# Kernel tuning notes

Hardware: AMD Instinct MI355X
Metric: run time of the kernel (lower is better)

The kernel has to match this reference:

```python
import jax, jax.numpy as jnp
import numpy as np

B, N, D = 32, 256, 3
NF, L = 16, 3


def _fully_connected(n):
    # Same ordering as connect_fully: for i in range(n) for j in range(n) if i != j
    a = np.repeat(np.arange(n), n)
    b = np.tile(np.arange(n), n)
    m = a != b
    return a[m].astype(np.int32), b[m].astype(np.int32)


def setup_inputs() -> dict:
    key = jax.random.key(0)
    ks = jax.random.split(key, 12)
    src, dst = _fully_connected(N)
    s = 0.1  # small param scale for numerical stability
    return {
        "xs": jax.random.normal(ks[0], (B, N, D), jnp.float32),
        "vs": jax.random.normal(ks[1], (B, N, D), jnp.float32),
        "charges": jax.random.normal(ks[2], (B * N, 1), jnp.float32),
        "W_in": s * jax.random.normal(ks[3], (1, NF), jnp.float32),
        "b_in": jnp.zeros((NF,), jnp.float32),
        "W_v": s * jax.random.normal(ks[4], (L, NF, 1), jnp.float32),
        "We1": s * jax.random.normal(ks[5], (L, 2 * NF + 1, NF), jnp.float32),
        "be1": jnp.zeros((L, NF), jnp.float32),
        "We2": s * jax.random.normal(ks[6], (L, NF, NF), jnp.float32),
        "be2": jnp.zeros((L, NF), jnp.float32),
        "Wx": s * jax.random.normal(ks[7], (L, NF, 1), jnp.float32),
        "Wh1": s * jax.random.normal(ks[8], (L, 2 * NF, NF), jnp.float32),
        "bh1": jnp.zeros((L, NF), jnp.float32),
        "src": jnp.asarray(src),
        "dst": jnp.asarray(dst),
    }


def reference(xs, vs, charges, W_in, b_in, W_v, We1, be1, We2, be2, Wx, Wh1, bh1, src, dst):
    b, n, d = xs.shape
    # node scalar features from charges (ndata['f'])
    h = jax.nn.relu(charges.reshape(b, n, 1) @ W_in + b_in)  # [B,N,nf]
    x = xs
    n_layers = We1.shape[0]
    for l in range(n_layers):
        # fully-connected edge gather + subtract (edata['d'])
        de = x[:, dst] - x[:, src]                         # [B,E,3]
        r2 = jnp.sum(de * de, axis=-1, keepdims=True)      # [B,E,1]
        e_in = jnp.concatenate([h[:, src], h[:, dst], r2], axis=-1)  # [B,E,2nf+1]
        m = jax.nn.relu(e_in @ We1[l] + be1[l])
        m = jax.nn.relu(m @ We2[l] + be2[l])               # [B,E,nf]
        w = m @ Wx[l]                                      # [B,E,1]
        # equivariant coordinate update: scatter-add edge vectors into dst nodes
        agg_x = jnp.zeros_like(x).at[:, dst].add(de * w) / (n - 1)
        x = x + agg_x + vs * (h @ W_v[l])                  # velocity term (ndata['vel'])
        m_agg = jnp.zeros_like(h).at[:, dst].add(m)        # [B,N,nf]
        h = h + jax.nn.relu(jnp.concatenate([h, m_agg], axis=-1) @ Wh1[l] + bh1[l])
    # OurDynamics returns (se3_out['1'] + xs).view(-1, n_dimension)
    return x.reshape(-1, d)
```

## Files before the change

kernel.cpp:

```cpp
#include <hip/hip_runtime.h>

#define BB 32
#define NN 256
#define NF 16

typedef _Float16 half4 __attribute__((ext_vector_type(4)));
typedef float f32x4 __attribute__((ext_vector_type(4)));

#define X0_OFF 0
#define X1_OFF 32768
#define H0_OFF 65536
#define H1_OFF 196608
#define SU0_OFF 327680
#define SV0_OFF 458752
#define SU1_OFF 589824
#define SV1_OFF 720896
#define SU2_OFF 851968
#define SV2_OFF 983040

__device__ __forceinline__ float dot4(float4 a, float4 b, float acc) {
    acc = fmaf(a.x, b.x, acc); acc = fmaf(a.y, b.y, acc);
    acc = fmaf(a.z, b.z, acc); acc = fmaf(a.w, b.w, acc);
    return acc;
}

__global__ __launch_bounds__(256)
void init_kernel(const float* __restrict__ xs, const float* __restrict__ charges,
                 const float* __restrict__ W_in, const float* __restrict__ b_in,
                 const float* __restrict__ We1, const float* __restrict__ be1,
                 float* __restrict__ x0, float* __restrict__ h0,
                 float* __restrict__ su0, float* __restrict__ sv0) {
    __shared__ float sWs[256], sWd[256];
    __shared__ __align__(16) float sh[16][NF];
    __shared__ float sb1[NF];
    const int tid = threadIdx.x;
    const size_t n0 = (size_t)blockIdx.x * 16;
    const int nl = tid >> 4;
    const int k  = tid & 15;
    sWs[tid] = We1[tid];
    sWd[tid] = We1[256 + tid];
    if (tid < NF) sb1[tid] = be1[tid];
    {
        const float c = charges[n0 + nl];
        const float hf = fmaxf(fmaf(c, W_in[k], b_in[k]), 0.f);
        sh[nl][k] = hf;
        h0[(n0 + nl) * NF + k] = hf;
    }
    if (tid < 64) {
        const int jd = tid >> 2, q = tid & 3;
        x0[(n0 + jd) * 4 + q] = (q < 3) ? xs[(n0 + jd) * 3 + q] : 0.f;
    }
    __syncthreads();
    {
        const float4* hn = (const float4*)&sh[nl][0];
        const float4 h0q = hn[0], h1q = hn[1], h2q = hn[2], h3q = hn[3];
        float u = 0.f, v = sb1[k];
#pragma unroll
        for (int q = 0; q < 4; ++q) {
            const float4 hq = (q == 0) ? h0q : (q == 1) ? h1q : (q == 2) ? h2q : h3q;
            u = fmaf(hq.x, sWs[(4 * q + 0) * NF + k], u);
            u = fmaf(hq.y, sWs[(4 * q + 1) * NF + k], u);
            u = fmaf(hq.z, sWs[(4 * q + 2) * NF + k], u);
            u = fmaf(hq.w, sWs[(4 * q + 3) * NF + k], u);
            v = fmaf(hq.x, sWd[(4 * q + 0) * NF + k], v);
            v = fmaf(hq.y, sWd[(4 * q + 1) * NF + k], v);
            v = fmaf(hq.z, sWd[(4 * q + 2) * NF + k], v);
            v = fmaf(hq.w, sWd[(4 * q + 3) * NF + k], v);
        }
        su0[(n0 + nl) * NF + k] = u;
        sv0[(n0 + nl) * NF + k] = v;
    }
}

__global__ __launch_bounds__(256)
void layer_kernel(const float* __restrict__ x_in, const float* __restrict__ h_in,
                  const float* __restrict__ su_in, const float* __restrict__ sv_in,
                  float* __restrict__ x_out, float* __restrict__ h_out,
                  float* __restrict__ su_out, float* __restrict__ sv_out,
                  const float* __restrict__ vs, const float* __restrict__ Wv_l,
                  const float* __restrict__ We1_l, const float* __restrict__ We2_l,
                  const float* __restrict__ be2_l, const float* __restrict__ Wx_l,
                  const float* __restrict__ Wh1_l, const float* __restrict__ bh1_l,
                  const float* __restrict__ We1_n, const float* __restrict__ be1_n,
                  int final_layer) {
    __shared__ __align__(16) float sSU[NN * NF];
    __shared__ __align__(16) float sX[NN * 4];
    __shared__ float sWh1s[512];
    __shared__ float sWa[256];
    __shared__ float sWb[256];
    __shared__ float sbe1n[NF];
    __shared__ float sh_new[8][NF + 1];
    __shared__ float sg[8][NF];

    const int tid  = threadIdx.x;
    const int b    = blockIdx.x >> 5;
    const int oct  = blockIdx.x & 31;
    const int n0l  = 8 * oct;
    const size_t n0 = (size_t)b * NN + n0l;
    const int w    = tid >> 6;
    const int lane = tid & 63;
    const int c    = lane & 15;
    const int g    = lane >> 4;

    sWh1s[tid]       = Wh1_l[tid];
    sWh1s[256 + tid] = Wh1_l[256 + tid];
    if (!final_layer) {
        const int f = tid >> 4, k = tid & 15;
        sWa[k * NF + f] = We1_n[tid];
        sWb[k * NF + f] = We1_n[256 + tid];
        if (tid < NF) sbe1n[tid] = be1_n[tid];
    }

    {
        const float4* gsu = (const float4*)(su_in + (size_t)b * NN * NF);
        float4* lsu = (float4*)sSU;
        lsu[tid]        = gsu[tid];
        lsu[256 + tid]  = gsu[256 + tid];
        lsu[512 + tid]  = gsu[512 + tid];
        lsu[768 + tid]  = gsu[768 + tid];
        const float4* gx = (const float4*)(x_in + (size_t)b * NN * 4);
        ((float4*)sX)[tid] = gx[tid];
    }
    __syncthreads();

    const int j0 = n0l + w, j1 = n0l + 4 + w;
    const float4 xj0 = *(const float4*)&sX[4 * j0];
    const float4 xj1 = *(const float4*)&sX[4 * j1];
    half4 afrag;
    afrag.x = (_Float16)We2_l[(4 * g + 0) * NF + c];
    afrag.y = (_Float16)We2_l[(4 * g + 1) * NF + c];
    afrag.z = (_Float16)We2_l[(4 * g + 2) * NF + c];
    afrag.w = (_Float16)We2_l[(4 * g + 3) * NF + c];
    const float4 v40  = *(const float4*)(sv_in + ((size_t)b * NN + j0) * NF + 4 * g);
    const float4 v41  = *(const float4*)(sv_in + ((size_t)b * NN + j1) * NF + 4 * g);
    const float4 wr4  = *(const float4*)(We1_l + 512 + 4 * g);
    const float4 be2f = *(const float4*)(be2_l + 4 * g);
    const float4 wxf  = *(const float4*)(Wx_l + 4 * g);
    f32x4 cb;
    cb.x = be2f.x; cb.y = be2f.y; cb.z = be2f.z; cb.w = be2f.w;

    float Sw0 = 0.f, Swx0 = 0.f, Swy0 = 0.f, Swz0 = 0.f;
    float Sw1 = 0.f, Swx1 = 0.f, Swy1 = 0.f, Swz1 = 0.f;
    float g00 = 0.f, g01 = 0.f, g02 = 0.f, g03 = 0.f;
    float g10 = 0.f, g11 = 0.f, g12 = 0.f, g13 = 0.f;

    const float* su_l = &sSU[c * NF + 4 * g];
    const float* x_l  = &sX[4 * c];

#pragma unroll 2
    for (int t = 0; t < 16; ++t) {
        const float4 u4  = *(const float4*)(su_l + 256 * t);
        const float4 xs4 = *(const float4*)(x_l + 64 * t);
        const int s = 16 * t + c;
        {
            const float dx = xj0.x - xs4.x, dy = xj0.y - xs4.y, dz = xj0.z - xs4.z;
            const float r2 = fmaf(dx, dx, fmaf(dy, dy, dz * dz));
            const float m0 = fmaxf(fmaf(r2, wr4.x, u4.x + v40.x), 0.f);
            const float m1 = fmaxf(fmaf(r2, wr4.y, u4.y + v40.y), 0.f);
            const float m2 = fmaxf(fmaf(r2, wr4.z, u4.z + v40.z), 0.f);
            const float m3 = fmaxf(fmaf(r2, wr4.w, u4.w + v40.w), 0.f);
            half4 bfrag;
            bfrag.x = (_Float16)m0; bfrag.y = (_Float16)m1;
            bfrag.z = (_Float16)m2; bfrag.w = (_Float16)m3;
            const f32x4 acc = __builtin_amdgcn_mfma_f32_16x16x16f16(afrag, bfrag, cb, 0, 0, 0);
            const float e0 = fmaxf(acc.x, 0.f);
            const float e1 = fmaxf(acc.y, 0.f);
            const float e2 = fmaxf(acc.z, 0.f);
            const float e3 = fmaxf(acc.w, 0.f);
            float wp = e0 * wxf.x;
            wp = fmaf(e1, wxf.y, wp);
            wp = fmaf(e2, wxf.z, wp);
            wp = fmaf(e3, wxf.w, wp);
            const float gsel = (s != j0) ? 1.f : 0.f;
            g00 = fmaf(e0, gsel, g00);
            g01 = fmaf(e1, gsel, g01);
            g02 = fmaf(e2, gsel, g02);
            g03 = fmaf(e3, gsel, g03);
            Sw0 += wp;
            Swx0 = fmaf(wp, xs4.x, Swx0);
            Swy0 = fmaf(wp, xs4.y, Swy0);
            Swz0 = fmaf(wp, xs4.z, Swz0);
        }
        {
            const float dx = xj1.x - xs4.x, dy = xj1.y - xs4.y, dz = xj1.z - xs4.z;
            const float r2 = fmaf(dx, dx, fmaf(dy, dy, dz * dz));
            const float m0 = fmaxf(fmaf(r2, wr4.x, u4.x + v41.x), 0.f);
            const float m1 = fmaxf(fmaf(r2, wr4.y, u4.y + v41.y), 0.f);
            const float m2 = fmaxf(fmaf(r2, wr4.z, u4.z + v41.z), 0.f);
            const float m3 = fmaxf(fmaf(r2, wr4.w, u4.w + v41.w), 0.f);
            half4 bfrag;
            bfrag.x = (_Float16)m0; bfrag.y = (_Float16)m1;
            bfrag.z = (_Float16)m2; bfrag.w = (_Float16)m3;
            const f32x4 acc = __builtin_amdgcn_mfma_f32_16x16x16f16(afrag, bfrag, cb, 0, 0, 0);
            const float e0 = fmaxf(acc.x, 0.f);
            const float e1 = fmaxf(acc.y, 0.f);
            const float e2 = fmaxf(acc.z, 0.f);
            const float e3 = fmaxf(acc.w, 0.f);
            float wp = e0 * wxf.x;
            wp = fmaf(e1, wxf.y, wp);
            wp = fmaf(e2, wxf.z, wp);
            wp = fmaf(e3, wxf.w, wp);
            const float gsel = (s != j1) ? 1.f : 0.f;
            g10 = fmaf(e0, gsel, g10);
            g11 = fmaf(e1, gsel, g11);
            g12 = fmaf(e2, gsel, g12);
            g13 = fmaf(e3, gsel, g13);
            Sw1 += wp;
            Swx1 = fmaf(wp, xs4.x, Swx1);
            Swy1 = fmaf(wp, xs4.y, Swy1);
            Swz1 = fmaf(wp, xs4.z, Swz1);
        }
    }

#pragma unroll
    for (int off = 1; off < 64; off <<= 1) {
        Sw0  += __shfl_xor(Sw0,  off, 64);  Sw1  += __shfl_xor(Sw1,  off, 64);
        Swx0 += __shfl_xor(Swx0, off, 64);  Swx1 += __shfl_xor(Swx1, off, 64);
        Swy0 += __shfl_xor(Swy0, off, 64);  Swy1 += __shfl_xor(Swy1, off, 64);
        Swz0 += __shfl_xor(Swz0, off, 64);  Swz1 += __shfl_xor(Swz1, off, 64);
    }
#pragma unroll
    for (int off = 1; off < 16; off <<= 1) {
        g00 += __shfl_xor(g00, off, 64);  g10 += __shfl_xor(g10, off, 64);
        g01 += __shfl_xor(g01, off, 64);  g11 += __shfl_xor(g11, off, 64);
        g02 += __shfl_xor(g02, off, 64);  g12 += __shfl_xor(g12, off, 64);
        g03 += __shfl_xor(g03, off, 64);  g13 += __shfl_xor(g13, off, 64);
    }
    if ((lane & 15) == 0) {
        *(float4*)&sg[w][4 * g]     = make_float4(g00, g01, g02, g03);
        *(float4*)&sg[w + 4][4 * g] = make_float4(g10, g11, g12, g13);
    }
    __syncthreads();

    const int is0 = (lane < 16);
    const int is1 = (lane >= 32 && lane < 48);
    if (is0 || is1) {
        const int f = lane & 15;
        const int slot = is0 ? w : (w + 4);
        const int jm   = is0 ? j0 : j1;
        const float SwS = is0 ? Sw0  : Sw1;
        const float SxS = is0 ? Swx0 : Swx1;
        const float SyS = is0 ? Swy0 : Swy1;
        const float SzS = is0 ? Swz0 : Swz1;
        const float4 xjm = is0 ? xj0 : xj1;
        const size_t nj = (size_t)b * NN + jm;
        float hd = bh1_l[f];
        float hv = 0.f;
#pragma unroll
        for (int k = 0; k < NF; ++k) {
            const float hjk = h_in[nj * NF + k];
            hd = fmaf(hjk, sWh1s[k * NF + f], hd);
            hv = fmaf(hjk, Wv_l[k], hv);
        }
#pragma unroll
        for (int k = 0; k < NF; ++k) {
            hd = fmaf(sg[slot][k], sWh1s[(NF + k) * NF + f], hd);
        }
        const float hnew = h_in[nj * NF + f] + fmaxf(hd, 0.f);
        sh_new[slot][f] = hnew;
        if (!final_layer) h_out[nj * NF + f] = hnew;
        if (f < 3) {
            const float xc = (f == 0) ? xjm.x : ((f == 1) ? xjm.y : xjm.z);
            const float Sc = (f == 0) ? SxS  : ((f == 1) ? SyS  : SzS);
            const float agg = (SwS * xc - Sc) * (1.f / 255.f);
            const float xnew = xc + agg + vs[nj * 3 + f] * hv;
            if (final_layer) x_out[nj * 3 + f] = xnew;
            else             x_out[nj * 4 + f] = xnew;
        }
        if (!final_layer && f == 3) x_out[nj * 4 + 3] = 0.f;
    }

    if (!final_layer) {
        __syncthreads();
        if (tid < 128) {
            const int jd = tid >> 4, k = tid & 15;
            float u = 0.f, v = sbe1n[k];
#pragma unroll
            for (int f = 0; f < NF; ++f) {
                const float hf = sh_new[jd][f];
                u = fmaf(hf, sWa[k * NF + f], u);
                v = fmaf(hf, sWb[k * NF + f], v);
            }
            su_out[(n0 + jd) * NF + k] = u;
            sv_out[(n0 + jd) * NF + k] = v;
        }
    }
}

extern "C" void kernel_launch(void* const* d_in, const int* in_sizes, int n_in,
                              void* d_out, int out_size, void* d_ws, size_t ws_size,
                              hipStream_t stream) {
    const float* xs      = (const float*)d_in[0];
    const float* vs      = (const float*)d_in[1];
    const float* charges = (const float*)d_in[2];
    const float* W_in    = (const float*)d_in[3];
    const float* b_in    = (const float*)d_in[4];
    const float* W_v     = (const float*)d_in[5];
    const float* We1     = (const float*)d_in[6];
    const float* be1     = (const float*)d_in[7];
    const float* We2     = (const float*)d_in[8];
    const float* be2     = (const float*)d_in[9];
    const float* Wx      = (const float*)d_in[10];
    const float* Wh1     = (const float*)d_in[11];
    const float* bh1     = (const float*)d_in[12];

    float* ws = (float*)d_ws;
    float* x0  = ws + X0_OFF;
    float* x1  = ws + X1_OFF;
    float* h0  = ws + H0_OFF;
    float* h1  = ws + H1_OFF;
    float* su0 = ws + SU0_OFF;
    float* sv0 = ws + SV0_OFF;
    float* su1 = ws + SU1_OFF;
    float* sv1 = ws + SV1_OFF;
    float* su2 = ws + SU2_OFF;
    float* sv2 = ws + SV2_OFF;
    float* out = (float*)d_out;

    hipLaunchKernelGGL(init_kernel, dim3(512), dim3(256), 0, stream,
                       xs, charges, W_in, b_in, We1, be1, x0, h0, su0, sv0);
    hipLaunchKernelGGL(layer_kernel, dim3(1024), dim3(256), 0, stream,
                       x0, h0, su0, sv0, x1, h1, su1, sv1,
                       vs, W_v + 0 * 16, We1 + 0 * 528, We2 + 0 * 256,
                       be2 + 0 * 16, Wx + 0 * 16, Wh1 + 0 * 512, bh1 + 0 * 16,
                       We1 + 1 * 528, be1 + 1 * 16, 0);
    hipLaunchKernelGGL(layer_kernel, dim3(1024), dim3(256), 0, stream,
                       x1, h1, su1, sv1, x0, h0, su2, sv2,
                       vs, W_v + 1 * 16, We1 + 1 * 528, We2 + 1 * 256,
                       be2 + 1 * 16, Wx + 1 * 16, Wh1 + 1 * 512, bh1 + 1 * 16,
                       We1 + 2 * 528, be1 + 2 * 16, 0);
    hipLaunchKernelGGL(layer_kernel, dim3(1024), dim3(256), 0, stream,
                       x0, h0, su2, sv2, out, h1, su1, sv1,
                       vs, W_v + 2 * 16, We1 + 2 * 528, We2 + 2 * 256,
                       be2 + 2 * 16, Wx + 2 * 16, Wh1 + 2 * 512, bh1 + 2 * 16,
                       We1 + 2 * 528, be1 + 2 * 16, 1);
}
```

Baseline: 132.8 us.

## Fuse init kernel into first layer kernel, recomputing node projections per block

```diff
diff --git a/kernel.cpp b/kernel.cpp
--- a/kernel.cpp
+++ b/kernel.cpp
@@ -1,93 +1,39 @@
 #include <hip/hip_runtime.h>
 
-#define BB 32
 #define NN 256
 #define NF 16
 
 typedef _Float16 half4 __attribute__((ext_vector_type(4)));
 typedef float f32x4 __attribute__((ext_vector_type(4)));
 
-#define X0_OFF 0
-#define X1_OFF 32768
-#define H0_OFF 65536
-#define H1_OFF 196608
-#define SU0_OFF 327680
-#define SV0_OFF 458752
-#define SU1_OFF 589824
-#define SV1_OFF 720896
-#define SU2_OFF 851968
-#define SV2_OFF 983040
-
-__device__ __forceinline__ float dot4(float4 a, float4 b, float acc) {
-    acc = fmaf(a.x, b.x, acc); acc = fmaf(a.y, b.y, acc);
-    acc = fmaf(a.z, b.z, acc); acc = fmaf(a.w, b.w, acc);
-    return acc;
-}
+#define XA_OFF 0
+#define XB_OFF 32768
+#define HA_OFF 65536
+#define HB_OFF 196608
+#define SUA_OFF 327680
+#define SVA_OFF 458752
+#define SUB_OFF 589824
+#define SVB_OFF 720896
 
 __global__ __launch_bounds__(256)
-void init_kernel(const float* __restrict__ xs, const float* __restrict__ charges,
-                 const float* __restrict__ W_in, const float* __restrict__ b_in,
-                 const float* __restrict__ We1, const float* __restrict__ be1,
-                 float* __restrict__ x0, float* __restrict__ h0,
-                 float* __restrict__ su0, float* __restrict__ sv0) {
-    __shared__ float sWs[256], sWd[256];
-    __shared__ __align__(16) float sh[16][NF];
-    __shared__ float sb1[NF];
-    const int tid = threadIdx.x;
-    const size_t n0 = (size_t)blockIdx.x * 16;
-    const int nl = tid >> 4;
-    const int k  = tid & 15;
-    sWs[tid] = We1[tid];
-    sWd[tid] = We1[256 + tid];
-    if (tid < NF) sb1[tid] = be1[tid];
-    {
-        const float c = charges[n0 + nl];
-        const float hf = fmaxf(fmaf(c, W_in[k], b_in[k]), 0.f);
-        sh[nl][k] = hf;
-        h0[(n0 + nl) * NF + k] = hf;
-    }
-    if (tid < 64) {
-        const int jd = tid >> 2, q = tid & 3;
-        x0[(n0 + jd) * 4 + q] = (q < 3) ? xs[(n0 + jd) * 3 + q] : 0.f;
-    }
-    __syncthreads();
-    {
-        const float4* hn = (const float4*)&sh[nl][0];
-        const float4 h0q = hn[0], h1q = hn[1], h2q = hn[2], h3q = hn[3];
-        float u = 0.f, v = sb1[k];
-#pragma unroll
-        for (int q = 0; q < 4; ++q) {
-            const float4 hq = (q == 0) ? h0q : (q == 1) ? h1q : (q == 2) ? h2q : h3q;
-            u = fmaf(hq.x, sWs[(4 * q + 0) * NF + k], u);
-            u = fmaf(hq.y, sWs[(4 * q + 1) * NF + k], u);
-            u = fmaf(hq.z, sWs[(4 * q + 2) * NF + k], u);
-            u = fmaf(hq.w, sWs[(4 * q + 3) * NF + k], u);
-            v = fmaf(hq.x, sWd[(4 * q + 0) * NF + k], v);
-            v = fmaf(hq.y, sWd[(4 * q + 1) * NF + k], v);
-            v = fmaf(hq.z, sWd[(4 * q + 2) * NF + k], v);
-            v = fmaf(hq.w, sWd[(4 * q + 3) * NF + k], v);
-        }
-        su0[(n0 + nl) * NF + k] = u;
-        sv0[(n0 + nl) * NF + k] = v;
-    }
-}
-
-__global__ __launch_bounds__(256)
-void layer_kernel(const float* __restrict__ x_in, const float* __restrict__ h_in,
-                  const float* __restrict__ su_in, const float* __restrict__ sv_in,
-                  float* __restrict__ x_out, float* __restrict__ h_out,
-                  float* __restrict__ su_out, float* __restrict__ sv_out,
-                  const float* __restrict__ vs, const float* __restrict__ Wv_l,
-                  const float* __restrict__ We1_l, const float* __restrict__ We2_l,
-                  const float* __restrict__ be2_l, const float* __restrict__ Wx_l,
-                  const float* __restrict__ Wh1_l, const float* __restrict__ bh1_l,
-                  const float* __restrict__ We1_n, const float* __restrict__ be1_n,
-                  int final_layer) {
+void layer0_kernel(const float* __restrict__ xs, const float* __restrict__ vs,
+                   const float* __restrict__ charges,
+                   const float* __restrict__ W_in, const float* __restrict__ b_in,
+                   const float* __restrict__ W_v, const float* __restrict__ We1_l,
+                   const float* __restrict__ be1_l, const float* __restrict__ We2_l,
+                   const float* __restrict__ be2_l, const float* __restrict__ Wx_l,
+                   const float* __restrict__ Wh1_l, const float* __restrict__ bh1_l,
+                   const float* __restrict__ We1_n, const float* __restrict__ be1_n,
+                   float* __restrict__ x_out, float* __restrict__ h_out,
+                   float* __restrict__ su_out, float* __restrict__ sv_out) {
     __shared__ __align__(16) float sSU[NN * NF];
     __shared__ __align__(16) float sX[NN * 4];
+    __shared__ __align__(16) float sHg[64 * NF];
+    __shared__ float sWs[256], sWd[256];
+    __shared__ __align__(16) float sSV8[8][NF];
+    __shared__ __align__(16) float sH8[8][NF + 1];
     __shared__ float sWh1s[512];
-    __shared__ float sWa[256];
-    __shared__ float sWb[256];
+    __shared__ float sWa[256], sWb[256];
     __shared__ float sbe1n[NF];
     __shared__ float sh_new[8][NF + 1];
     __shared__ float sg[8][NF];
@@ -102,26 +48,71 @@
     const int c    = lane & 15;
     const int g    = lane >> 4;
 
+    sWs[tid] = We1_l[tid];
+    sWd[tid] = We1_l[256 + tid];
     sWh1s[tid]       = Wh1_l[tid];
     sWh1s[256 + tid] = Wh1_l[256 + tid];
-    if (!final_layer) {
-        const int f = tid >> 4, k = tid & 15;
-        sWa[k * NF + f] = We1_n[tid];
-        sWb[k * NF + f] = We1_n[256 + tid];
+    {
+        const int f = tid >> 4, kk = tid & 15;
+        sWa[kk * NF + f] = We1_n[tid];
+        sWb[kk * NF + f] = We1_n[256 + tid];
         if (tid < NF) sbe1n[tid] = be1_n[tid];
     }
-
     {
-        const float4* gsu = (const float4*)(su_in + (size_t)b * NN * NF);
-        float4* lsu = (float4*)sSU;
-        lsu[tid]        = gsu[tid];
-        lsu[256 + tid]  = gsu[256 + tid];
-        lsu[512 + tid]  = gsu[512 + tid];
-        lsu[768 + tid]  = gsu[768 + tid];
-        const float4* gx = (const float4*)(x_in + (size_t)b * NN * 4);
-        ((float4*)sX)[tid] = gx[tid];
-    }
-    __syncthreads();
+        const size_t base = ((size_t)b * NN + tid) * 3;
+        sX[tid * 4 + 0] = xs[base + 0];
+        sX[tid * 4 + 1] = xs[base + 1];
+        sX[tid * 4 + 2] = xs[base + 2];
+        sX[tid * 4 + 3] = 0.f;
+    }
+
+    const int nl = tid >> 4, k = tid & 15;
+    const float win  = W_in[k];
+    const float bin  = b_in[k];
+    const float be1k = be1_l[k];
+    const int i0 = n0l >> 6;
+    const int r0 = (n0l & 63) >> 4;
+    const int halfsel = (n0l >> 3) & 1;
+    const int own = ((nl >> 3) == halfsel);
+#pragma unroll
+    for (int i = 0; i < 4; ++i) {
+#pragma unroll
+        for (int r = 0; r < 4; ++r) {
+            const float cq = charges[(size_t)b * NN + 64 * i + 16 * r + nl];
+            const float hf = fmaxf(fmaf(cq, win, bin), 0.f);
+            sHg[(16 * r + nl) * NF + k] = hf;
+            if (i == i0 && r == r0 && own) sH8[nl & 7][k] = hf;
+        }
+        __syncthreads();
+#pragma unroll
+        for (int r = 0; r < 4; ++r) {
+            const float4* hn = (const float4*)&sHg[(16 * r + nl) * NF];
+            const float4 h0q = hn[0], h1q = hn[1], h2q = hn[2], h3q = hn[3];
+            float u = 0.f;
+#pragma unroll
+            for (int q = 0; q < 4; ++q) {
+                const float4 hq = (q == 0) ? h0q : (q == 1) ? h1q : (q == 2) ? h2q : h3q;
+                u = fmaf(hq.x, sWs[(4 * q + 0) * NF + k], u);
+                u = fmaf(hq.y, sWs[(4 * q + 1) * NF + k], u);
+                u = fmaf(hq.z, sWs[(4 * q + 2) * NF + k], u);
+                u = fmaf(hq.w, sWs[(4 * q + 3) * NF + k], u);
+            }
+            sSU[(64 * i + 16 * r + nl) * NF + k] = u;
+            if (i == i0 && r == r0 && own) {
+                float v = be1k;
+#pragma unroll
+                for (int q = 0; q < 4; ++q) {
+                    const float4 hq = (q == 0) ? h0q : (q == 1) ? h1q : (q == 2) ? h2q : h3q;
+                    v = fmaf(hq.x, sWd[(4 * q + 0) * NF + k], v);
+                    v = fmaf(hq.y, sWd[(4 * q + 1) * NF + k], v);
+                    v = fmaf(hq.z, sWd[(4 * q + 2) * NF + k], v);
+                    v = fmaf(hq.w, sWd[(4 * q + 3) * NF + k], v);
+                }
+                sSV8[nl & 7][k] = v;
+            }
+        }
+        __syncthreads();
+    }
 
     const int j0 = n0l + w, j1 = n0l + 4 + w;
     const float4 xj0 = *(const float4*)&sX[4 * j0];
@@ -131,8 +122,8 @@
     afrag.y = (_Float16)We2_l[(4 * g + 1) * NF + c];
     afrag.z = (_Float16)We2_l[(4 * g + 2) * NF + c];
     afrag.w = (_Float16)We2_l[(4 * g + 3) * NF + c];
-    const float4 v40  = *(const float4*)(sv_in + ((size_t)b * NN + j0) * NF + 4 * g);
-    const float4 v41  = *(const float4*)(sv_in + ((size_t)b * NN + j1) * NF + 4 * g);
+    const float4 v40 = *(const float4*)&sSV8[w][4 * g];
+    const float4 v41 = *(const float4*)&sSV8[4 + w][4 * g];
     const float4 wr4  = *(const float4*)(We1_l + 512 + 4 * g);
     const float4 be2f = *(const float4*)(be2_l + 4 * g);
     const float4 wxf  = *(const float4*)(Wx_l + 4 * g);
@@ -247,6 +238,217 @@
         float hd = bh1_l[f];
         float hv = 0.f;
 #pragma unroll
+        for (int kk = 0; kk < NF; ++kk) {
+            const float hjk = sH8[slot][kk];
+            hd = fmaf(hjk, sWh1s[kk * NF + f], hd);
+            hv = fmaf(hjk, W_v[kk], hv);
+        }
+#pragma unroll
+        for (int kk = 0; kk < NF; ++kk) {
+            hd = fmaf(sg[slot][kk], sWh1s[(NF + kk) * NF + f], hd);
+        }
+        const float hnew = sH8[slot][f] + fmaxf(hd, 0.f);
+        sh_new[slot][f] = hnew;
+        h_out[nj * NF + f] = hnew;
+        if (f < 3) {
+            const float xc = (f == 0) ? xjm.x : ((f == 1) ? xjm.y : xjm.z);
+            const float Sc = (f == 0) ? SxS  : ((f == 1) ? SyS  : SzS);
+            const float agg = (SwS * xc - Sc) * (1.f / 255.f);
+            const float xnew = xc + agg + vs[nj * 3 + f] * hv;
+            x_out[nj * 4 + f] = xnew;
+        }
+        if (f == 3) x_out[nj * 4 + 3] = 0.f;
+    }
+
+    __syncthreads();
+    if (tid < 128) {
+        const int jd = tid >> 4, kk = tid & 15;
+        float u = 0.f, v = sbe1n[kk];
+#pragma unroll
+        for (int f = 0; f < NF; ++f) {
+            const float hf = sh_new[jd][f];
+            u = fmaf(hf, sWa[kk * NF + f], u);
+            v = fmaf(hf, sWb[kk * NF + f], v);
+        }
+        su_out[(n0 + jd) * NF + kk] = u;
+        sv_out[(n0 + jd) * NF + kk] = v;
+    }
+}
+
+__global__ __launch_bounds__(256)
+void layer_kernel(const float* __restrict__ x_in, const float* __restrict__ h_in,
+                  const float* __restrict__ su_in, const float* __restrict__ sv_in,
+                  float* __restrict__ x_out, float* __restrict__ h_out,
+                  float* __restrict__ su_out, float* __restrict__ sv_out,
+                  const float* __restrict__ vs, const float* __restrict__ Wv_l,
+                  const float* __restrict__ We1_l, const float* __restrict__ We2_l,
+                  const float* __restrict__ be2_l, const float* __restrict__ Wx_l,
+                  const float* __restrict__ Wh1_l, const float* __restrict__ bh1_l,
+                  const float* __restrict__ We1_n, const float* __restrict__ be1_n,
+                  int final_layer) {
+    __shared__ __align__(16) float sSU[NN * NF];
+    __shared__ __align__(16) float sX[NN * 4];
+    __shared__ float sWh1s[512];
+    __shared__ float sWa[256];
+    __shared__ float sWb[256];
+    __shared__ float sbe1n[NF];
+    __shared__ float sh_new[8][NF + 1];
+    __shared__ float sg[8][NF];
+
+    const int tid  = threadIdx.x;
+    const int b    = blockIdx.x >> 5;
+    const int oct  = blockIdx.x & 31;
+    const int n0l  = 8 * oct;
+    const size_t n0 = (size_t)b * NN + n0l;
+    const int w    = tid >> 6;
+    const int lane = tid & 63;
+    const int c    = lane & 15;
+    const int g    = lane >> 4;
+
+    sWh1s[tid]       = Wh1_l[tid];
+    sWh1s[256 + tid] = Wh1_l[256 + tid];
+    if (!final_layer) {
+        const int f = tid >> 4, k = tid & 15;
+        sWa[k * NF + f] = We1_n[tid];
+        sWb[k * NF + f] = We1_n[256 + tid];
+        if (tid < NF) sbe1n[tid] = be1_n[tid];
+    }
+    {
+        const float4* gsu = (const float4*)(su_in + (size_t)b * NN * NF);
+        float4* lsu = (float4*)sSU;
+        lsu[tid]        = gsu[tid];
+        lsu[256 + tid]  = gsu[256 + tid];
+        lsu[512 + tid]  = gsu[512 + tid];
+        lsu[768 + tid]  = gsu[768 + tid];
+        const float4* gx = (const float4*)(x_in + (size_t)b * NN * 4);
+        ((float4*)sX)[tid] = gx[tid];
+    }
+    __syncthreads();
+
+    const int j0 = n0l + w, j1 = n0l + 4 + w;
+    const float4 xj0 = *(const float4*)&sX[4 * j0];
+    const float4 xj1 = *(const float4*)&sX[4 * j1];
+    half4 afrag;
+    afrag.x = (_Float16)We2_l[(4 * g + 0) * NF + c];
+    afrag.y = (_Float16)We2_l[(4 * g + 1) * NF + c];
+    afrag.z = (_Float16)We2_l[(4 * g + 2) * NF + c];
+    afrag.w = (_Float16)We2_l[(4 * g + 3) * NF + c];
+    const float4 v40  = *(const float4*)(sv_in + ((size_t)b * NN + j0) * NF + 4 * g);
+    const float4 v41  = *(const float4*)(sv_in + ((size_t)b * NN + j1) * NF + 4 * g);
+    const float4 wr4  = *(const float4*)(We1_l + 512 + 4 * g);
+    const float4 be2f = *(const float4*)(be2_l + 4 * g);
+    const float4 wxf  = *(const float4*)(Wx_l + 4 * g);
+    f32x4 cb;
+    cb.x = be2f.x; cb.y = be2f.y; cb.z = be2f.z; cb.w = be2f.w;
+
+    float Sw0 = 0.f, Swx0 = 0.f, Swy0 = 0.f, Swz0 = 0.f;
+    float Sw1 = 0.f, Swx1 = 0.f, Swy1 = 0.f, Swz1 = 0.f;
+    float g00 = 0.f, g01 = 0.f, g02 = 0.f, g03 = 0.f;
+    float g10 = 0.f, g11 = 0.f, g12 = 0.f, g13 = 0.f;
+
+    const float* su_l = &sSU[c * NF + 4 * g];
+    const float* x_l  = &sX[4 * c];
+
+#pragma unroll 2
+    for (int t = 0; t < 16; ++t) {
+        const float4 u4  = *(const float4*)(su_l + 256 * t);
+        const float4 xs4 = *(const float4*)(x_l + 64 * t);
+        const int s = 16 * t + c;
+        {
+            const float dx = xj0.x - xs4.x, dy = xj0.y - xs4.y, dz = xj0.z - xs4.z;
+            const float r2 = fmaf(dx, dx, fmaf(dy, dy, dz * dz));
+            const float m0 = fmaxf(fmaf(r2, wr4.x, u4.x + v40.x), 0.f);
+            const float m1 = fmaxf(fmaf(r2, wr4.y, u4.y + v40.y), 0.f);
+            const float m2 = fmaxf(fmaf(r2, wr4.z, u4.z + v40.z), 0.f);
+            const float m3 = fmaxf(fmaf(r2, wr4.w, u4.w + v40.w), 0.f);
+            half4 bfrag;
+            bfrag.x = (_Float16)m0; bfrag.y = (_Float16)m1;
+            bfrag.z = (_Float16)m2; bfrag.w = (_Float16)m3;
+            const f32x4 acc = __builtin_amdgcn_mfma_f32_16x16x16f16(afrag, bfrag, cb, 0, 0, 0);
+            const float e0 = fmaxf(acc.x, 0.f);
+            const float e1 = fmaxf(acc.y, 0.f);
+            const float e2 = fmaxf(acc.z, 0.f);
+            const float e3 = fmaxf(acc.w, 0.f);
+            float wp = e0 * wxf.x;
+            wp = fmaf(e1, wxf.y, wp);
+            wp = fmaf(e2, wxf.z, wp);
+            wp = fmaf(e3, wxf.w, wp);
+            const float gsel = (s != j0) ? 1.f : 0.f;
+            g00 = fmaf(e0, gsel, g00);
+            g01 = fmaf(e1, gsel, g01);
+            g02 = fmaf(e2, gsel, g02);
+            g03 = fmaf(e3, gsel, g03);
+            Sw0 += wp;
+            Swx0 = fmaf(wp, xs4.x, Swx0);
+            Swy0 = fmaf(wp, xs4.y, Swy0);
+            Swz0 = fmaf(wp, xs4.z, Swz0);
+        }
+        {
+            const float dx = xj1.x - xs4.x, dy = xj1.y - xs4.y, dz = xj1.z - xs4.z;
+            const float r2 = fmaf(dx, dx, fmaf(dy, dy, dz * dz));
+            const float m0 = fmaxf(fmaf(r2, wr4.x, u4.x + v41.x), 0.f);
+            const float m1 = fmaxf(fmaf(r2, wr4.y, u4.y + v41.y), 0.f);
+            const float m2 = fmaxf(fmaf(r2, wr4.z, u4.z + v41.z), 0.f);
+            const float m3 = fmaxf(fmaf(r2, wr4.w, u4.w + v41.w), 0.f);
+            half4 bfrag;
+            bfrag.x = (_Float16)m0; bfrag.y = (_Float16)m1;
+            bfrag.z = (_Float16)m2; bfrag.w = (_Float16)m3;
+            const f32x4 acc = __builtin_amdgcn_mfma_f32_16x16x16f16(afrag, bfrag, cb, 0, 0, 0);
+            const float e0 = fmaxf(acc.x, 0.f);
+            const float e1 = fmaxf(acc.y, 0.f);
+            const float e2 = fmaxf(acc.z, 0.f);
+            const float e3 = fmaxf(acc.w, 0.f);
+            float wp = e0 * wxf.x;
+            wp = fmaf(e1, wxf.y, wp);
+            wp = fmaf(e2, wxf.z, wp);
+            wp = fmaf(e3, wxf.w, wp);
+            const float gsel = (s != j1) ? 1.f : 0.f;
+            g10 = fmaf(e0, gsel, g10);
+            g11 = fmaf(e1, gsel, g11);
+            g12 = fmaf(e2, gsel, g12);
+            g13 = fmaf(e3, gsel, g13);
+            Sw1 += wp;
+            Swx1 = fmaf(wp, xs4.x, Swx1);
+            Swy1 = fmaf(wp, xs4.y, Swy1);
+            Swz1 = fmaf(wp, xs4.z, Swz1);
+        }
+    }
+
+#pragma unroll
+    for (int off = 1; off < 64; off <<= 1) {
+        Sw0  += __shfl_xor(Sw0,  off, 64);  Sw1  += __shfl_xor(Sw1,  off, 64);
+        Swx0 += __shfl_xor(Swx0, off, 64);  Swx1 += __shfl_xor(Swx1, off, 64);
+        Swy0 += __shfl_xor(Swy0, off, 64);  Swy1 += __shfl_xor(Swy1, off, 64);
+        Swz0 += __shfl_xor(Swz0, off, 64);  Swz1 += __shfl_xor(Swz1, off, 64);
+    }
+#pragma unroll
+    for (int off = 1; off < 16; off <<= 1) {
+        g00 += __shfl_xor(g00, off, 64);  g10 += __shfl_xor(g10, off, 64);
+        g01 += __shfl_xor(g01, off, 64);  g11 += __shfl_xor(g11, off, 64);
+        g02 += __shfl_xor(g02, off, 64);  g12 += __shfl_xor(g12, off, 64);
+        g03 += __shfl_xor(g03, off, 64);  g13 += __shfl_xor(g13, off, 64);
+    }
+    if ((lane & 15) == 0) {
+        *(float4*)&sg[w][4 * g]     = make_float4(g00, g01, g02, g03);
+        *(float4*)&sg[w + 4][4 * g] = make_float4(g10, g11, g12, g13);
+    }
+    __syncthreads();
+
+    const int is0 = (lane < 16);
+    const int is1 = (lane >= 32 && lane < 48);
+    if (is0 || is1) {
+        const int f = lane & 15;
+        const int slot = is0 ? w : (w + 4);
+        const int jm   = is0 ? j0 : j1;
+        const float SwS = is0 ? Sw0  : Sw1;
+        const float SxS = is0 ? Swx0 : Swx1;
+        const float SyS = is0 ? Swy0 : Swy1;
+        const float SzS = is0 ? Swz0 : Swz1;
+        const float4 xjm = is0 ? xj0 : xj1;
+        const size_t nj = (size_t)b * NN + jm;
+        float hd = bh1_l[f];
+        float hv = 0.f;
+#pragma unroll
         for (int k = 0; k < NF; ++k) {
             const float hjk = h_in[nj * NF + k];
             hd = fmaf(hjk, sWh1s[k * NF + f], hd);
@@ -305,32 +507,29 @@
     const float* bh1     = (const float*)d_in[12];
 
     float* ws = (float*)d_ws;
-    float* x0  = ws + X0_OFF;
-    float* x1  = ws + X1_OFF;
-    float* h0  = ws + H0_OFF;
-    float* h1  = ws + H1_OFF;
-    float* su0 = ws + SU0_OFF;
-    float* sv0 = ws + SV0_OFF;
-    float* su1 = ws + SU1_OFF;
-    float* sv1 = ws + SV1_OFF;
-    float* su2 = ws + SU2_OFF;
-    float* sv2 = ws + SV2_OFF;
+    float* xA  = ws + XA_OFF;
+    float* xB  = ws + XB_OFF;
+    float* hA  = ws + HA_OFF;
+    float* hB  = ws + HB_OFF;
+    float* suA = ws + SUA_OFF;
+    float* svA = ws + SVA_OFF;
+    float* suB = ws + SUB_OFF;
+    float* svB = ws + SVB_OFF;
     float* out = (float*)d_out;
 
-    hipLaunchKernelGGL(init_kernel, dim3(512), dim3(256), 0, stream,
-                       xs, charges, W_in, b_in, We1, be1, x0, h0, su0, sv0);
+    hipLaunchKernelGGL(layer0_kernel, dim3(1024), dim3(256), 0, stream,
+                       xs, vs, charges, W_in, b_in,
+                       W_v + 0 * 16, We1 + 0 * 528, be1 + 0 * 16, We2 + 0 * 256,
+                       be2 + 0 * 16, Wx + 0 * 16, Wh1 + 0 * 512, bh1 + 0 * 16,
+                       We1 + 1 * 528, be1 + 1 * 16,
+                       xA, hA, suA, svA);
     hipLaunchKernelGGL(layer_kernel, dim3(1024), dim3(256), 0, stream,
-                       x0, h0, su0, sv0, x1, h1, su1, sv1,
-                       vs, W_v + 0 * 16, We1 + 0 * 528, We2 + 0 * 256,
-                       be2 + 0 * 16, Wx + 0 * 16, Wh1 + 0 * 512, bh1 + 0 * 16,
-                       We1 + 1 * 528, be1 + 1 * 16, 0);
-    hipLaunchKernelGGL(layer_kernel, dim3(1024), dim3(256), 0, stream,
-                       x1, h1, su1, sv1, x0, h0, su2, sv2,
+                       xA, hA, suA, svA, xB, hB, suB, svB,
                        vs, W_v + 1 * 16, We1 + 1 * 528, We2 + 1 * 256,
                        be2 + 1 * 16, Wx + 1 * 16, Wh1 + 1 * 512, bh1 + 1 * 16,
                        We1 + 2 * 528, be1 + 2 * 16, 0);
     hipLaunchKernelGGL(layer_kernel, dim3(1024), dim3(256), 0, stream,
-                       x0, h0, su2, sv2, out, h1, su1, sv1,
+                       xB, hB, suB, svB, out, hA, suA, svA,
                        vs, W_v + 2 * 16, We1 + 2 * 528, We2 + 2 * 256,
                        be2 + 2 * 16, Wx + 2 * 16, Wh1 + 2 * 512, bh1 + 2 * 16,
                        We1 + 2 * 528, be1 + 2 * 16, 1);
```

New measurement: 131.8 us. No clear change (-0.7%).
